# Performance work log

Measured on AMD Instinct MI355X. Metric: run time of the kernel, lower is better.

Reference implementation:

```python
import jax, jax.numpy as jnp
import numpy as np

N_CLASSES = 80
SEG_LEN = 512          # boxes per class (uniform segments)
H = 128                # hidden_size
DH = 2 * H             # decoder hidden (= concat of bidirectional encoder final hiddens)
EMB = 32               # decoder_input_dim
SOS, EOS = 2, 3


def _gru_cell(x, h, Wih, Whh, bih, bhh):
    # PyTorch GRU cell math. x:(in,), h:(hid,), Wih:(3*hid,in), Whh:(3*hid,hid)
    gi = Wih @ x + bih
    gh = Whh @ h + bhh
    i_r, i_z, i_n = jnp.split(gi, 3)
    h_r, h_z, h_n = jnp.split(gh, 3)
    r = jax.nn.sigmoid(i_r + h_r)
    z = jax.nn.sigmoid(i_z + h_z)
    n = jnp.tanh(i_n + r * h_n)
    return (1.0 - z) * n + z * h


def _gru_seq(xs, h0, Wih, Whh, bih, bhh):
    # xs: (T, in); returns final hidden (hid,) and all hiddens (T, hid)
    def step(h, x):
        h2 = _gru_cell(x, h, Wih, Whh, bih, bhh)
        return h2, h2
    hT, hs = jax.lax.scan(step, h0, xs)
    return hT, hs

# vmap over the 80 classes (per-class weights)
_run_gru = jax.vmap(_gru_seq, in_axes=(0, 0, 0, 0, 0, 0))


def setup_inputs() -> dict:
    key = jax.random.key(0)
    ks = jax.random.split(key, 32)
    N = N_CLASSES * SEG_LEN
    s = 0.05
    inp = {
        "feat": jax.random.normal(ks[0], (N, 1024), jnp.float32),
        "score": jax.random.uniform(ks[1], (N, 1), jnp.float32),
        "box": jax.random.uniform(ks[2], (N, 4), jnp.float32),
        "origin_score": jax.random.uniform(ks[3], (N, 91), jnp.float32),
        "labels": jax.random.randint(ks[4], (N,), 0, 2, jnp.int64),
        "weights": jax.random.uniform(ks[5], (N,), jnp.float32),
        "unique_class": jnp.ones((N_CLASSES,), jnp.int64),
        "unique_class_len": jnp.arange(N_CLASSES + 1, dtype=jnp.int64) * SEG_LEN,
        # shared linears
        "appear_W": jax.random.normal(ks[6], (H, 1024), jnp.float32) * s,
        "appear_b": jnp.zeros((H,), jnp.float32),
        "featlin_W": jax.random.normal(ks[7], (H, H + 96), jnp.float32) * s,
        "featlin_b": jnp.zeros((H,), jnp.float32),
        # per-class bidirectional encoder GRUs
        "enc_Wih_f": jax.random.normal(ks[8], (N_CLASSES, 3 * H, H), jnp.float32) * s,
        "enc_Whh_f": jax.random.normal(ks[9], (N_CLASSES, 3 * H, H), jnp.float32) * s,
        "enc_bih_f": jnp.zeros((N_CLASSES, 3 * H), jnp.float32),
        "enc_bhh_f": jnp.zeros((N_CLASSES, 3 * H), jnp.float32),
        "enc_Wih_b": jax.random.normal(ks[10], (N_CLASSES, 3 * H, H), jnp.float32) * s,
        "enc_Whh_b": jax.random.normal(ks[11], (N_CLASSES, 3 * H, H), jnp.float32) * s,
        "enc_bih_b": jnp.zeros((N_CLASSES, 3 * H), jnp.float32),
        "enc_bhh_b": jnp.zeros((N_CLASSES, 3 * H), jnp.float32),
        # decoder
        "dec_emb": jax.random.normal(ks[12], (4, EMB), jnp.float32) * s,
        "dec_Wih": jax.random.normal(ks[13], (N_CLASSES, 3 * DH, EMB), jnp.float32) * s,
        "dec_Whh": jax.random.normal(ks[14], (N_CLASSES, 3 * DH, DH), jnp.float32) * s,
        "dec_bih": jnp.zeros((N_CLASSES, 3 * DH), jnp.float32),
        "dec_bhh": jnp.zeros((N_CLASSES, 3 * DH), jnp.float32),
        "out_W": jax.random.normal(ks[15], (4, DH), jnp.float32) * s,
        "out_b": jnp.zeros((4,), jnp.float32),
    }
    return inp


def reference(feat, score, box, origin_score, labels, weights, unique_class,
              unique_class_len, appear_W, appear_b, featlin_W, featlin_b,
              enc_Wih_f, enc_Whh_f, enc_bih_f, enc_bhh_f,
              enc_Wih_b, enc_Whh_b, enc_bih_b, enc_bhh_b,
              dec_emb, dec_Wih, dec_Whh, dec_bih, dec_bhh, out_W, out_b):
    # --- shared feature encoding ---
    x = jax.nn.relu(feat @ appear_W.T + appear_b)                    # (N, H)
    allf = jnp.concatenate([x, score, box, origin_score], axis=1)    # (N, H+96)
    enc_feat = jax.nn.relu(allf @ featlin_W.T + featlin_b)           # (N, H)

    # --- per-class bidirectional encoder (uniform segments) ---
    seg = enc_feat.reshape(N_CLASSES, SEG_LEN, H)
    eos = jnp.ones((N_CLASSES, 1, H), enc_feat.dtype)                # encoder_EOS = ones
    enc_in = jnp.concatenate([seg, eos], axis=1)                     # (80, L+1, H)
    h0 = jnp.zeros((N_CLASSES, H), enc_feat.dtype)
    h_f, _ = _run_gru(enc_in, h0, enc_Wih_f, enc_Whh_f, enc_bih_f, enc_bhh_f)
    h_b, _ = _run_gru(enc_in[:, ::-1], h0, enc_Wih_b, enc_Whh_b, enc_bih_b, enc_bhh_b)
    dec_h0 = jnp.concatenate([h_f, h_b], axis=-1)                    # (80, 2H)

    # --- per-class decoder with teacher forcing (SOS then gold labels) ---
    emb = dec_emb[labels].reshape(N_CLASSES, SEG_LEN, EMB)
    sos = jnp.broadcast_to(dec_emb[SOS], (N_CLASSES, 1, EMB))
    dec_in = jnp.concatenate([sos, emb], axis=1)                     # (80, L+1, EMB)
    _, dec_hs = _run_gru(dec_in, dec_h0, dec_Wih, dec_Whh, dec_bih, dec_bhh)

    logits = dec_hs.reshape(-1, DH) @ out_W.T + out_b                # (80*(L+1), 4)
    output = jax.nn.log_softmax(logits, axis=-1)
    return output, labels, weights
```

## Files before the change

### kernel.cpp

```cpp
#include <hip/hip_runtime.h>


typedef __fp16 h2v __attribute__((ext_vector_type(2)));
typedef __fp16 h8 __attribute__((ext_vector_type(8)));

__device__ __forceinline__ h2v pk2(float a, float b) {
  return __builtin_amdgcn_cvt_pkrtz(a, b);
}
__device__ __forceinline__ unsigned h2u(h2v h) { return __builtin_bit_cast(unsigned, h); }
__device__ __forceinline__ h2v u2h(unsigned u) { return __builtin_bit_cast(h2v, u); }
__device__ __forceinline__ float fdot2f(h2v a, h2v b, float c) {
  return __builtin_amdgcn_fdot2(a, b, c, false);
}
__device__ __forceinline__ float sigf(float x) { return 1.f / (1.f + __expf(-x)); }
__device__ __forceinline__ float tanhfast(float x) { return 2.f / (1.f + __expf(-2.f * x)) - 1.f; }

__device__ __forceinline__ h8 pack8(float4 a, float4 b) {
  h2v p0 = pk2(a.x, a.y), p1 = pk2(a.z, a.w), p2 = pk2(b.x, b.y), p3 = pk2(b.z, b.w);
  return (h8){p0[0], p0[1], p1[0], p1[1], p2[0], p2[1], p3[0], p3[1]};
}

#define SL(V, j) (__builtin_shufflevector((V), (V), 2 * (j), 2 * (j) + 1))

template <int CTRL>
__device__ __forceinline__ float dppadd(float acc, float v) {
  int r = __builtin_amdgcn_update_dpp(0, __float_as_int(v), CTRL, 0xF, 0xF, true);
  return acc + __int_as_float(r);
}
__device__ __forceinline__ float swz4add(float acc, float v) {
  return acc + __int_as_float(__builtin_amdgcn_ds_swizzle(__float_as_int(v), 0x101F));
}

__device__ __forceinline__ float reduce8s(float p0, float p1, float p2, float p3,
                                          float p4, float p5, float p6, float p7) {
  p0 = dppadd<0xB1>(p0, p1);
  p2 = dppadd<0xB1>(p2, p3);
  p4 = dppadd<0xB1>(p4, p5);
  p6 = dppadd<0xB1>(p6, p7);
  p0 = dppadd<0x4E>(p0, p2);
  p4 = dppadd<0x4E>(p4, p6);
  p0 = swz4add(p0, p4);
  p0 = dppadd<0x128>(p0, p0);
  return p0;
}

__device__ __forceinline__ float dot4(h8 V, h2v a0, h2v a1, h2v a2, h2v a3, float acc) {
  acc = fdot2f(SL(V, 0), a0, acc);
  acc = fdot2f(SL(V, 1), a1, acc);
  acc = fdot2f(SL(V, 2), a2, acc);
  acc = fdot2f(SL(V, 3), a3, acc);
  return acc;
}

__global__ void k_fill_misc(const float* __restrict__ score, const float* __restrict__ box,
                            const float* __restrict__ orig, float* __restrict__ allf) {
  int i = blockIdx.x * blockDim.x + threadIdx.x;
  if (i >= 40960 * 96) return;
  int row = i / 96, k = i - row * 96;
  float v;
  if (k == 0) v = score[row];
  else if (k < 5) v = box[row * 4 + (k - 1)];
  else v = orig[(size_t)row * 91 + (k - 5)];
  allf[(size_t)row * 224 + 128 + k] = v;
}

__global__ __launch_bounds__(256) void k_gemm_appear(
    const float* __restrict__ A, const float* __restrict__ W,
    const float* __restrict__ bias, float* __restrict__ allf) {
  __shared__ float As[32][68];
  __shared__ float Ws[32][132];
  const int tid = threadIdx.x;
  const int tx = tid & 15, ty = tid >> 4;
  const int r0 = blockIdx.x * 64;
  const int lr = tid >> 3;
  const int lk = (tid & 7) * 4;
  float acc[4][8];
#pragma unroll
  for (int i = 0; i < 4; ++i)
#pragma unroll
    for (int j = 0; j < 8; ++j) acc[i][j] = 0.f;

  for (int k0 = 0; k0 < 1024; k0 += 32) {
#pragma unroll
    for (int i = 0; i < 2; ++i) {
      int rr = lr + i * 32;
      float4 v = *(const float4*)(A + (size_t)(r0 + rr) * 1024 + k0 + lk);
      As[lk + 0][rr] = v.x; As[lk + 1][rr] = v.y; As[lk + 2][rr] = v.z; As[lk + 3][rr] = v.w;
    }
#pragma unroll
    for (int i = 0; i < 4; ++i) {
      int wr = lr + i * 32;
      float4 v = *(const float4*)(W + (size_t)wr * 1024 + k0 + lk);
      Ws[lk + 0][wr] = v.x; Ws[lk + 1][wr] = v.y; Ws[lk + 2][wr] = v.z; Ws[lk + 3][wr] = v.w;
    }
    __syncthreads();
#pragma unroll
    for (int kk = 0; kk < 32; ++kk) {
      float4 a = *(const float4*)&As[kk][ty * 4];
      float4 w0 = *(const float4*)&Ws[kk][tx * 8];
      float4 w1 = *(const float4*)&Ws[kk][tx * 8 + 4];
      float av[4] = {a.x, a.y, a.z, a.w};
      float wv[8] = {w0.x, w0.y, w0.z, w0.w, w1.x, w1.y, w1.z, w1.w};
#pragma unroll
      for (int i = 0; i < 4; ++i)
#pragma unroll
        for (int j = 0; j < 8; ++j) acc[i][j] = fmaf(av[i], wv[j], acc[i][j]);
    }
    __syncthreads();
  }
#pragma unroll
  for (int i = 0; i < 4; ++i) {
    int row = r0 + ty * 4 + i;
#pragma unroll
    for (int j = 0; j < 8; ++j) {
      int col = tx * 8 + j;
      float v = acc[i][j] + bias[col];
      allf[(size_t)row * 224 + col] = fmaxf(v, 0.f);
    }
  }
}

__global__ __launch_bounds__(256) void k_gemm_featlin(
    const float* __restrict__ A, const float* __restrict__ W,
    const float* __restrict__ bias, unsigned* __restrict__ encf2) {
  __shared__ float As[32][68];
  __shared__ float Ws[32][132];
  const int tid = threadIdx.x;
  const int tx = tid & 15, ty = tid >> 4;
  const int r0 = blockIdx.x * 64;
  const int lr = tid >> 3;
  const int lk = (tid & 7) * 4;
  float acc[4][8];
#pragma unroll
  for (int i = 0; i < 4; ++i)
#pragma unroll
    for (int j = 0; j < 8; ++j) acc[i][j] = 0.f;

  for (int k0 = 0; k0 < 224; k0 += 32) {
#pragma unroll
    for (int i = 0; i < 2; ++i) {
      int rr = lr + i * 32;
      float4 v = *(const float4*)(A + (size_t)(r0 + rr) * 224 + k0 + lk);
      As[lk + 0][rr] = v.x; As[lk + 1][rr] = v.y; As[lk + 2][rr] = v.z; As[lk + 3][rr] = v.w;
    }
#pragma unroll
    for (int i = 0; i < 4; ++i) {
      int wr = lr + i * 32;
      float4 v = *(const float4*)(W + (size_t)wr * 224 + k0 + lk);
      Ws[lk + 0][wr] = v.x; Ws[lk + 1][wr] = v.y; Ws[lk + 2][wr] = v.z; Ws[lk + 3][wr] = v.w;
    }
    __syncthreads();
#pragma unroll
    for (int kk = 0; kk < 32; ++kk) {
      float4 a = *(const float4*)&As[kk][ty * 4];
      float4 w0 = *(const float4*)&Ws[kk][tx * 8];
      float4 w1 = *(const float4*)&Ws[kk][tx * 8 + 4];
      float av[4] = {a.x, a.y, a.z, a.w};
      float wv[8] = {w0.x, w0.y, w0.z, w0.w, w1.x, w1.y, w1.z, w1.w};
#pragma unroll
      for (int i = 0; i < 4; ++i)
#pragma unroll
        for (int j = 0; j < 8; ++j) acc[i][j] = fmaf(av[i], wv[j], acc[i][j]);
    }
    __syncthreads();
  }
#pragma unroll
  for (int i = 0; i < 4; ++i) {
    int row = r0 + ty * 4 + i;
    unsigned* orow = encf2 + (size_t)row * 64;
#pragma unroll
    for (int p = 0; p < 4; ++p) {
      int col = tx * 8 + 2 * p;
      float a = fmaxf(acc[i][2 * p] + bias[col], 0.f);
      float b = fmaxf(acc[i][2 * p + 1] + bias[col + 1], 0.f);
      orow[tx * 4 + p] = h2u(pk2(a, b));
    }
  }
}

__global__ __launch_bounds__(256) void k_dec_gi(
    const float* __restrict__ Wih, const float* __restrict__ bih,
    const float* __restrict__ emb, float* __restrict__ gi) {
  __shared__ float e[4][32];
  const int c = blockIdx.x, tid = threadIdx.x;
  if (tid < 128) e[tid >> 5][tid & 31] = emb[tid];
  __syncthreads();
#pragma unroll
  for (int i = 0; i < 3; ++i) {
    int r = tid + i * 256;
    const float* w = Wih + ((size_t)c * 768 + r) * 32;
    float b = bih[(size_t)c * 768 + r];
    float a0 = b, a1 = b, a2 = b, a3 = b;
#pragma unroll
    for (int k = 0; k < 32; ++k) {
      float wv = w[k];
      a0 = fmaf(wv, e[0][k], a0);
      a1 = fmaf(wv, e[1][k], a1);
      a2 = fmaf(wv, e[2][k], a2);
      a3 = fmaf(wv, e[3][k], a3);
    }
    gi[((size_t)c * 4 + 0) * 768 + r] = a0;
    gi[((size_t)c * 4 + 1) * 768 + r] = a1;
    gi[((size_t)c * 4 + 2) * 768 + r] = a2;
    gi[((size_t)c * 4 + 3) * 768 + r] = a3;
  }
}

#define OCC_PAD_WORDS 21504

#define ENCROW(k)                                                                   \
  h8 ci_##k, ch_##k, sg_##k;                                                        \
  {                                                                                 \
    int vc = 32 * w + 8 * q + ((k) ^ mw);                                           \
    const float4* pi = (const float4*)(Wih + (size_t)vc * 128 + 8 * m);             \
    ci_##k = pack8(pi[0], pi[1]);                                                   \
    __builtin_amdgcn_sched_barrier(0);                                              \
    const float4* ph = (const float4*)(Whh + (size_t)vc * 128 + 8 * m);             \
    ch_##k = pack8(ph[0], ph[1]);                                                   \
    __builtin_amdgcn_sched_barrier(0);                                              \
    int s = (w < 4) ? vc : (vc - 128);                                              \
    const float* sb =                                                               \
        (w < 4) ? (Wih + (size_t)(256 + s) * 128) : (Whh + (size_t)(256 + s) * 128);\
    const float4* ps = (const float4*)(sb + 8 * m);                                 \
    sg_##k = pack8(ps[0], ps[1]);                                                   \
    __builtin_amdgcn_sched_barrier(0);                                              \
  }

#define EDOTC(k) dot4(ci_##k, x0, x1, x2, x3, dot4(ch_##k, g0, g1, g2, g3, 0.f))
#define EDOTS(k) dot4(sg_##k, s0, s1, s2, s3, 0.f)

__global__ __launch_bounds__(512) void k_enc_gru(
    const unsigned* __restrict__ encf2,
    const float* __restrict__ WihF, const float* __restrict__ WhhF,
    const float* __restrict__ bihF, const float* __restrict__ bhhF,
    const float* __restrict__ WihB, const float* __restrict__ WhhB,
    const float* __restrict__ bihB, const float* __restrict__ bhhB,
    float* __restrict__ dec_h0) {
  const int blk = blockIdx.x;
  const int c = blk >> 1, dir = blk & 1;
  const int tid = threadIdx.x;
  const int w = tid >> 6, l = tid & 63, q = l >> 4, m = l & 15, mw = m & 7;

  const float* Wih = (dir ? WihB : WihF) + (size_t)c * 384 * 128;
  const float* Whh = (dir ? WhhB : WhhF) + (size_t)c * 384 * 128;
  const float* bih = (dir ? bihB : bihF) + (size_t)c * 384;
  const float* bhh = (dir ? bhhB : bhhF) + (size_t)c * 384;

  __shared__ __align__(16) unsigned x2s[2][64];
  __shared__ __align__(16) unsigned h2s[64];
  __shared__ float aBuf[512];
  __shared__ float occ_pad[OCC_PAD_WORDS];
  if (tid == 0) ((volatile float*)occ_pad)[0] = 0.f;

  ENCROW(0) ENCROW(1) ENCROW(2) ENCROW(3)
  ENCROW(4) ENCROW(5) ENCROW(6) ENCROW(7)

  float bown;
  int ownIdx;
  if (m < 8) {
    int vo = 32 * w + 8 * q + m;
    bown = bih[vo] + bhh[vo];
    ownIdx = vo;
  } else {
    int so = (w < 4) ? (32 * w + 8 * q + mw) : (32 * (w - 4) + 8 * q + mw);
    bown = (w < 4) ? bih[256 + so] : bhh[256 + so];
    ownIdx = (w < 4) ? (256 + so) : (384 + so);
  }

  if (tid < 64) h2s[tid] = 0u;
  if (tid >= 448) {
    int lane = tid - 448;
    x2s[0][lane] = (dir == 0) ? encf2[((size_t)c * 512 + 0) * 64 + lane] : 0x3C003C00u;
  }
  float hreg = 0.f;
  __syncthreads();

  for (int t = 0; t <= 512; ++t) {
    unsigned xpre = 0;
    if (tid >= 448 && t < 512) {
      int tn = t + 1, lane = tid - 448;
      int row = (dir == 0) ? ((tn < 512) ? tn : -1) : (512 - tn);
      xpre = (row < 0) ? 0x3C003C00u : encf2[((size_t)c * 512 + row) * 64 + lane];
    }
    uint4 xv = ((const uint4*)&x2s[t & 1][0])[m];
    uint4 hv = ((const uint4*)&h2s[0])[m];
    h2v x0 = u2h(xv.x), x1 = u2h(xv.y), x2 = u2h(xv.z), x3 = u2h(xv.w);
    h2v g0 = u2h(hv.x), g1 = u2h(hv.y), g2 = u2h(hv.z), g3 = u2h(hv.w);
    float pA = reduce8s(EDOTC(0), EDOTC(1), EDOTC(2), EDOTC(3),
                        EDOTC(4), EDOTC(5), EDOTC(6), EDOTC(7));
    h2v s0 = (w < 4) ? x0 : g0, s1 = (w < 4) ? x1 : g1;
    h2v s2 = (w < 4) ? x2 : g2, s3 = (w < 4) ? x3 : g3;
    float pB = reduce8s(EDOTS(0), EDOTS(1), EDOTS(2), EDOTS(3),
                        EDOTS(4), EDOTS(5), EDOTS(6), EDOTS(7));
    aBuf[ownIdx] = ((m < 8) ? pA : pB) + bown;
    __syncthreads();
    if (tid < 128) {
      float r = sigf(aBuf[tid]);
      float z = sigf(aBuf[128 + tid]);
      float nn = tanhfast(aBuf[256 + tid] + r * aBuf[384 + tid]);
      float hn = (1.f - z) * nn + z * hreg;
      hreg = hn;
      float other = __shfl_xor(hn, 1, 64);
      if ((tid & 1) == 0) h2s[tid >> 1] = h2u(pk2(hn, other));
    } else if (tid >= 448 && t < 512) {
      x2s[(t + 1) & 1][tid - 448] = xpre;
    }
    __syncthreads();
  }
  if (tid < 128) dec_h0[(size_t)c * 256 + dir * 128 + tid] = hreg;
}

#define DECROW(kc, k)                                                               \
  h8 wA##kc##_##k, wB##kc##_##k;                                                    \
  {                                                                                 \
    int row = 64 * w + 16 * q + 8 * (kc) + ((k) ^ mw);                              \
    const float4* src = (const float4*)(Whh + ((size_t)c * 768 + row) * 256 + 16 * m);\
    float4 v0 = src[0], v1 = src[1];                                                \
    wA##kc##_##k = pack8(v0, v1);                                                   \
    __builtin_amdgcn_sched_barrier(0);                                              \
    float4 v2 = src[2], v3 = src[3];                                                \
    wB##kc##_##k = pack8(v2, v3);                                                   \
    __builtin_amdgcn_sched_barrier(0);                                              \
  }

#define DDOT(kc, k)                                                        \
  (fdot2f(SL(wB##kc##_##k, 3), g7,                                         \
   fdot2f(SL(wB##kc##_##k, 2), g6,                                         \
   fdot2f(SL(wB##kc##_##k, 1), g5,                                         \
   fdot2f(SL(wB##kc##_##k, 0), g4,                                         \
   fdot2f(SL(wA##kc##_##k, 3), g3,                                         \
   fdot2f(SL(wA##kc##_##k, 2), g2,                                         \
   fdot2f(SL(wA##kc##_##k, 1), g1,                                         \
   fdot2f(SL(wA##kc##_##k, 0), g0, 0.f)))))))))

__global__ __launch_bounds__(768) void k_dec_gru(
    const float* __restrict__ Whh, const float* __restrict__ bhh,
    const float* __restrict__ gi, const float* __restrict__ h0,
    const int* __restrict__ labels,
    const float* __restrict__ outW, const float* __restrict__ outB,
    float* __restrict__ out) {
  const int c = blockIdx.x, tid = threadIdx.x;
  const int w = tid >> 6, l = tid & 63, q = l >> 4, m = l & 15, mw = m & 7;

  __shared__ __align__(16) unsigned h2s[128];
  __shared__ float aBuf[768];
  __shared__ float gisf[2304];
  __shared__ float owsh[1024];
  __shared__ int labs[513];
  __shared__ float red[4][4];
  __shared__ float occ_pad[OCC_PAD_WORDS];
  if (tid == 0) ((volatile float*)occ_pad)[0] = 0.f;

  DECROW(0, 0) DECROW(0, 1) DECROW(0, 2) DECROW(0, 3)
  DECROW(0, 4) DECROW(0, 5) DECROW(0, 6) DECROW(0, 7)
  DECROW(1, 0) DECROW(1, 1) DECROW(1, 2) DECROW(1, 3)
  DECROW(1, 4) DECROW(1, 5) DECROW(1, 6) DECROW(1, 7)

  float bown = bhh[(size_t)c * 768 + 64 * w + l];

  for (int i = tid; i < 2304; i += 768) gisf[i] = gi[(size_t)c * 4 * 768 + i];
  for (int i = tid; i < 1024; i += 768) owsh[i] = outW[i];
  if (tid < 512) labs[tid + 1] = labels[(size_t)c * 512 + tid];
  if (tid == 512) labs[0] = 2;
  float b0 = outB[0], b1 = outB[1], b2 = outB[2], b3 = outB[3];
  float hreg = 0.f;
  if (tid < 256) {
    hreg = h0[(size_t)c * 256 + tid];
    float other = __shfl_xor(hreg, 1, 64);
    if ((tid & 1) == 0) h2s[tid >> 1] = h2u(pk2(hreg, other));
  }
  __syncthreads();

  for (int t = 0; t <= 512; ++t) {
    const uint4* hp = (const uint4*)(&h2s[0]);
    uint4 ha = hp[2 * m], hb = hp[2 * m + 1];
    h2v g0 = u2h(ha.x), g1 = u2h(ha.y), g2 = u2h(ha.z), g3 = u2h(ha.w);
    h2v g4 = u2h(hb.x), g5 = u2h(hb.y), g6 = u2h(hb.z), g7 = u2h(hb.w);
    float pc0 = reduce8s(DDOT(0, 0), DDOT(0, 1), DDOT(0, 2), DDOT(0, 3),
                         DDOT(0, 4), DDOT(0, 5), DDOT(0, 6), DDOT(0, 7));
    float pc1 = reduce8s(DDOT(1, 0), DDOT(1, 1), DDOT(1, 2), DDOT(1, 3),
                         DDOT(1, 4), DDOT(1, 5), DDOT(1, 6), DDOT(1, 7));
    aBuf[64 * w + l] = ((m < 8) ? pc0 : pc1) + bown;
    __syncthreads();
    if (tid < 256) {
      int sel = labs[t];
      const float* gsel = &gisf[sel * 768];
      float r = sigf(gsel[tid] + aBuf[tid]);
      float z = sigf(gsel[256 + tid] + aBuf[256 + tid]);
      float nn = tanhfast(gsel[512 + tid] + r * aBuf[512 + tid]);
      float hn = (1.f - z) * nn + z * hreg;
      hreg = hn;
      float other = __shfl_xor(hn, 1, 64);
      if ((tid & 1) == 0) h2s[tid >> 1] = h2u(pk2(hn, other));
      float p0 = owsh[tid] * hn, p1 = owsh[256 + tid] * hn;
      float p2 = owsh[512 + tid] * hn, p3 = owsh[768 + tid] * hn;
#pragma unroll
      for (int off = 32; off > 0; off >>= 1) {
        p0 += __shfl_xor(p0, off, 64);
        p1 += __shfl_xor(p1, off, 64);
        p2 += __shfl_xor(p2, off, 64);
        p3 += __shfl_xor(p3, off, 64);
      }
      if ((tid & 63) == 0) {
        int ww = tid >> 6;
        red[ww][0] = p0; red[ww][1] = p1; red[ww][2] = p2; red[ww][3] = p3;
      }
    }
    __syncthreads();
    if (tid == 0) {
      float l0 = red[0][0] + red[1][0] + red[2][0] + red[3][0] + b0;
      float l1 = red[0][1] + red[1][1] + red[2][1] + red[3][1] + b1;
      float l2 = red[0][2] + red[1][2] + red[2][2] + red[3][2] + b2;
      float l3 = red[0][3] + red[1][3] + red[2][3] + red[3][3] + b3;
      float mm = fmaxf(fmaxf(l0, l1), fmaxf(l2, l3));
      float s = __expf(l0 - mm) + __expf(l1 - mm) + __expf(l2 - mm) + __expf(l3 - mm);
      float lse = mm + __logf(s);
      float* o = out + ((size_t)c * 513 + t) * 4;
      o[0] = l0 - lse; o[1] = l1 - lse; o[2] = l2 - lse; o[3] = l3 - lse;
    }
  }
}

__global__ void k_passthrough(const int* __restrict__ labels,
                              const float* __restrict__ weights,
                              float* __restrict__ out) {
  int i = blockIdx.x * blockDim.x + threadIdx.x;
  if (i < 40960) {
    out[164160 + i] = (float)labels[i];
    out[164160 + 40960 + i] = weights[i];
  }
}

extern "C" void kernel_launch(void* const* d_in, const int* in_sizes, int n_in,
                              void* d_out, int out_size, void* d_ws, size_t ws_size,
                              hipStream_t stream) {
  (void)in_sizes; (void)n_in; (void)out_size; (void)ws_size;
  const float* feat = (const float*)d_in[0];
  const float* score = (const float*)d_in[1];
  const float* box = (const float*)d_in[2];
  const float* orig = (const float*)d_in[3];
  const int* labels = (const int*)d_in[4];
  const float* weights = (const float*)d_in[5];
  const float* appear_W = (const float*)d_in[8];
  const float* appear_b = (const float*)d_in[9];
  const float* featlin_W = (const float*)d_in[10];
  const float* featlin_b = (const float*)d_in[11];
  const float* eWihF = (const float*)d_in[12];
  const float* eWhhF = (const float*)d_in[13];
  const float* ebihF = (const float*)d_in[14];
  const float* ebhhF = (const float*)d_in[15];
  const float* eWihB = (const float*)d_in[16];
  const float* eWhhB = (const float*)d_in[17];
  const float* ebihB = (const float*)d_in[18];
  const float* ebhhB = (const float*)d_in[19];
  const float* dec_emb = (const float*)d_in[20];
  const float* dWih = (const float*)d_in[21];
  const float* dWhh = (const float*)d_in[22];
  const float* dbih = (const float*)d_in[23];
  const float* dbhh = (const float*)d_in[24];
  const float* outW = (const float*)d_in[25];
  const float* outB = (const float*)d_in[26];
  float* out = (float*)d_out;

  char* ws = (char*)d_ws;
  float* allf = (float*)ws;
  unsigned* encf2 = (unsigned*)(ws + (size_t)40960 * 224 * 4);
  float* dec_h0 = (float*)(ws + (size_t)40960 * 224 * 4 + (size_t)40960 * 64 * 4);
  float* dec_gi = dec_h0 + 80 * 256;

  k_fill_misc<<<15360, 256, 0, stream>>>(score, box, orig, allf);
  k_gemm_appear<<<640, 256, 0, stream>>>(feat, appear_W, appear_b, allf);
  k_gemm_featlin<<<640, 256, 0, stream>>>(allf, featlin_W, featlin_b, encf2);
  k_dec_gi<<<80, 256, 0, stream>>>(dWih, dbih, dec_emb, dec_gi);
  k_enc_gru<<<160, 512, 0, stream>>>(encf2, eWihF, eWhhF, ebihF, ebhhF,
                                     eWihB, eWhhB, ebihB, ebhhB, dec_h0);
  k_dec_gru<<<80, 768, 0, stream>>>(dWhh, dbhh, dec_gi, dec_h0, labels, outW, outB, out);
  k_passthrough<<<160, 256, 0, stream>>>(labels, weights, out);
}
```

Baseline: 1.657 ms.

## Stream pre-packed fp16 decoder weights from global instead of holding in registers

Adds a pre-pass kernel that converts the decoder recurrent weights to fp16 and lays them out per thread for coalesced loads. The decoder kernel then no longer keeps all weights in registers; it streams them from global or L2 every step with a rolling prefetch buffer of four slots. Barriers now wait only on LDS counters, so the weight loads stay in flight across barriers. The shared-memory occupancy padding is also removed. This trades register pressure for memory traffic on every step, which risks exposing load latency on the sequential critical path.

```diff
diff --git a/kernel.cpp b/kernel.cpp
--- a/kernel.cpp
+++ b/kernel.cpp
@@ -206,7 +206,23 @@
   }
 }
 
-#define OCC_PAD_WORDS 21504
+__global__ __launch_bounds__(768) void k_pack_dec(
+    const float* __restrict__ Whh, uint4* __restrict__ wpk) {
+  const int c = blockIdx.x >> 5, ic = blockIdx.x & 31;
+  const int tid = threadIdx.x;
+  const int w = tid >> 6, l = tid & 63, q = l >> 4, m = l & 15, mw = m & 7;
+  const int kc = ic >> 4, kk = (ic >> 1) & 7, half = ic & 1;
+  const int row = 64 * w + 16 * q + 8 * kc + (kk ^ mw);
+  const float* src = Whh + ((size_t)c * 768 + row) * 256 + 16 * m + 8 * half;
+  float4 a = *(const float4*)(src);
+  float4 b = *(const float4*)(src + 4);
+  uint4 o;
+  o.x = h2u(pk2(a.x, a.y));
+  o.y = h2u(pk2(a.z, a.w));
+  o.z = h2u(pk2(b.x, b.y));
+  o.w = h2u(pk2(b.z, b.w));
+  wpk[((size_t)c * 32 + ic) * 768 + tid] = o;
+}
 
 #define ENCROW(k)                                                                   \
   h8 ci_##k, ch_##k, sg_##k;                                                        \
@@ -249,8 +265,6 @@
   __shared__ __align__(16) unsigned x2s[2][64];
   __shared__ __align__(16) unsigned h2s[64];
   __shared__ float aBuf[512];
-  __shared__ float occ_pad[OCC_PAD_WORDS];
-  if (tid == 0) ((volatile float*)occ_pad)[0] = 0.f;
 
   ENCROW(0) ENCROW(1) ENCROW(2) ENCROW(3)
   ENCROW(4) ENCROW(5) ENCROW(6) ENCROW(7)
@@ -310,37 +324,38 @@
   if (tid < 128) dec_h0[(size_t)c * 256 + dir * 128 + tid] = hreg;
 }
 
-#define DECROW(kc, k)                                                               \
-  h8 wA##kc##_##k, wB##kc##_##k;                                                    \
-  {                                                                                 \
-    int row = 64 * w + 16 * q + 8 * (kc) + ((k) ^ mw);                              \
-    const float4* src = (const float4*)(Whh + ((size_t)c * 768 + row) * 256 + 16 * m);\
-    float4 v0 = src[0], v1 = src[1];                                                \
-    wA##kc##_##k = pack8(v0, v1);                                                   \
-    __builtin_amdgcn_sched_barrier(0);                                              \
-    float4 v2 = src[2], v3 = src[3];                                                \
-    wB##kc##_##k = pack8(v2, v3);                                                   \
-    __builtin_amdgcn_sched_barrier(0);                                              \
-  }
-
-#define DDOT(kc, k)                                                        \
-  (fdot2f(SL(wB##kc##_##k, 3), g7,                                         \
-   fdot2f(SL(wB##kc##_##k, 2), g6,                                         \
-   fdot2f(SL(wB##kc##_##k, 1), g5,                                         \
-   fdot2f(SL(wB##kc##_##k, 0), g4,                                         \
-   fdot2f(SL(wA##kc##_##k, 3), g3,                                         \
-   fdot2f(SL(wA##kc##_##k, 2), g2,                                         \
-   fdot2f(SL(wA##kc##_##k, 1), g1,                                         \
-   fdot2f(SL(wA##kc##_##k, 0), g0, 0.f)))))))))
+#define CONS(sa, sb, dst)                                   \
+  {                                                         \
+    float a_ = 0.f;                                         \
+    a_ = fdot2f(u2h((sa).x), g0, a_);                       \
+    a_ = fdot2f(u2h((sa).y), g1, a_);                       \
+    a_ = fdot2f(u2h((sa).z), g2, a_);                       \
+    a_ = fdot2f(u2h((sa).w), g3, a_);                       \
+    a_ = fdot2f(u2h((sb).x), g4, a_);                       \
+    a_ = fdot2f(u2h((sb).y), g5, a_);                       \
+    a_ = fdot2f(u2h((sb).z), g6, a_);                       \
+    a_ = fdot2f(u2h((sb).w), g7, a_);                       \
+    dst = a_;                                               \
+  }
+
+#define DITER(P, J, D)                                      \
+  CONS(bA##P, bB##P, D);                                    \
+  bA##P = wp[((2 * (J) + 8) & 31) * 768];                   \
+  bB##P = wp[((2 * (J) + 9) & 31) * 768];
+
+#define BAR_LGKM()                                          \
+  asm volatile("s_waitcnt lgkmcnt(0)" ::: "memory");        \
+  __builtin_amdgcn_s_barrier();                             \
+  asm volatile("" ::: "memory");
 
 __global__ __launch_bounds__(768) void k_dec_gru(
-    const float* __restrict__ Whh, const float* __restrict__ bhh,
+    const uint4* __restrict__ wpk, const float* __restrict__ bhh,
     const float* __restrict__ gi, const float* __restrict__ h0,
     const int* __restrict__ labels,
     const float* __restrict__ outW, const float* __restrict__ outB,
     float* __restrict__ out) {
   const int c = blockIdx.x, tid = threadIdx.x;
-  const int w = tid >> 6, l = tid & 63, q = l >> 4, m = l & 15, mw = m & 7;
+  const int w = tid >> 6, l = tid & 63, m = l & 15;
 
   __shared__ __align__(16) unsigned h2s[128];
   __shared__ float aBuf[768];
@@ -348,16 +363,14 @@
   __shared__ float owsh[1024];
   __shared__ int labs[513];
   __shared__ float red[4][4];
-  __shared__ float occ_pad[OCC_PAD_WORDS];
-  if (tid == 0) ((volatile float*)occ_pad)[0] = 0.f;
-
-  DECROW(0, 0) DECROW(0, 1) DECROW(0, 2) DECROW(0, 3)
-  DECROW(0, 4) DECROW(0, 5) DECROW(0, 6) DECROW(0, 7)
-  DECROW(1, 0) DECROW(1, 1) DECROW(1, 2) DECROW(1, 3)
-  DECROW(1, 4) DECROW(1, 5) DECROW(1, 6) DECROW(1, 7)
+
+  const uint4* wp = wpk + (size_t)c * 32 * 768 + tid;
+  uint4 bA0 = wp[0 * 768], bB0 = wp[1 * 768];
+  uint4 bA1 = wp[2 * 768], bB1 = wp[3 * 768];
+  uint4 bA2 = wp[4 * 768], bB2 = wp[5 * 768];
+  uint4 bA3 = wp[6 * 768], bB3 = wp[7 * 768];
 
   float bown = bhh[(size_t)c * 768 + 64 * w + l];
-
   for (int i = tid; i < 2304; i += 768) gisf[i] = gi[(size_t)c * 4 * 768 + i];
   for (int i = tid; i < 1024; i += 768) owsh[i] = outW[i];
   if (tid < 512) labs[tid + 1] = labels[(size_t)c * 512 + tid];
@@ -376,12 +389,15 @@
     uint4 ha = hp[2 * m], hb = hp[2 * m + 1];
     h2v g0 = u2h(ha.x), g1 = u2h(ha.y), g2 = u2h(ha.z), g3 = u2h(ha.w);
     h2v g4 = u2h(hb.x), g5 = u2h(hb.y), g6 = u2h(hb.z), g7 = u2h(hb.w);
-    float pc0 = reduce8s(DDOT(0, 0), DDOT(0, 1), DDOT(0, 2), DDOT(0, 3),
-                         DDOT(0, 4), DDOT(0, 5), DDOT(0, 6), DDOT(0, 7));
-    float pc1 = reduce8s(DDOT(1, 0), DDOT(1, 1), DDOT(1, 2), DDOT(1, 3),
-                         DDOT(1, 4), DDOT(1, 5), DDOT(1, 6), DDOT(1, 7));
+    float s0, s1, s2, s3, s4, s5, s6, s7;
+    DITER(0, 0, s0) DITER(1, 1, s1) DITER(2, 2, s2) DITER(3, 3, s3)
+    DITER(0, 4, s4) DITER(1, 5, s5) DITER(2, 6, s6) DITER(3, 7, s7)
+    float pc0 = reduce8s(s0, s1, s2, s3, s4, s5, s6, s7);
+    DITER(0, 8, s0) DITER(1, 9, s1) DITER(2, 10, s2) DITER(3, 11, s3)
+    DITER(0, 12, s4) DITER(1, 13, s5) DITER(2, 14, s6) DITER(3, 15, s7)
+    float pc1 = reduce8s(s0, s1, s2, s3, s4, s5, s6, s7);
     aBuf[64 * w + l] = ((m < 8) ? pc0 : pc1) + bown;
-    __syncthreads();
+    BAR_LGKM();
     if (tid < 256) {
       int sel = labs[t];
       const float* gsel = &gisf[sel * 768];
@@ -406,7 +422,7 @@
         red[ww][0] = p0; red[ww][1] = p1; red[ww][2] = p2; red[ww][3] = p3;
       }
     }
-    __syncthreads();
+    BAR_LGKM();
     if (tid == 0) {
       float l0 = red[0][0] + red[1][0] + red[2][0] + red[3][0] + b0;
       float l1 = red[0][1] + red[1][1] + red[2][1] + red[3][1] + b1;
@@ -467,13 +483,15 @@
   unsigned* encf2 = (unsigned*)(ws + (size_t)40960 * 224 * 4);
   float* dec_h0 = (float*)(ws + (size_t)40960 * 224 * 4 + (size_t)40960 * 64 * 4);
   float* dec_gi = dec_h0 + 80 * 256;
+  uint4* wpack = (uint4*)allf;
 
   k_fill_misc<<<15360, 256, 0, stream>>>(score, box, orig, allf);
   k_gemm_appear<<<640, 256, 0, stream>>>(feat, appear_W, appear_b, allf);
   k_gemm_featlin<<<640, 256, 0, stream>>>(allf, featlin_W, featlin_b, encf2);
+  k_pack_dec<<<80 * 32, 768, 0, stream>>>(dWhh, wpack);
   k_dec_gi<<<80, 256, 0, stream>>>(dWih, dbih, dec_emb, dec_gi);
   k_enc_gru<<<160, 512, 0, stream>>>(encf2, eWihF, eWhhF, ebihF, ebhhF,
                                      eWihB, eWhhB, ebihB, ebhhB, dec_h0);
-  k_dec_gru<<<80, 768, 0, stream>>>(dWhh, dbhh, dec_gi, dec_h0, labels, outW, outB, out);
+  k_dec_gru<<<80, 768, 0, stream>>>(wpack, dbhh, dec_gi, dec_h0, labels, outW, outB, out);
   k_passthrough<<<160, 256, 0, stream>>>(labels, weights, out);
 }
```

After: 1.819 ms. +9.7%, slower.
